# Kernel tuning notes

Hardware: AMD Instinct MI355X
Metric: run time of the kernel (lower is better)

Reference implementation:

```python
import jax, jax.numpy as jnp
import numpy as np

# Dimensions: D must equal C_CHUNK**2 (original code's view+transpose requires it)
D = 4096        # flattened input dim per sample
C_CHUNK = 64    # chunk_size (rows of G per chunk)
N_CHUNKS = D // C_CHUNK  # = 64
H = 512         # hidden dim of forward_func MLP
C_OUT = 8       # output classes of forward_func
B = 8           # batch size (state_batch has 2*B rows)
EPS_G = 1e-4    # metric regularizer (constant under grad)


def setup_inputs() -> dict:
    key = jax.random.key(0)
    ks = jax.random.split(key, 6)
    t = jax.random.uniform(ks[0], (1,), dtype=jnp.float32)
    state_batch = jax.random.normal(ks[1], (2 * B, D), dtype=jnp.float32)
    x0_batch = jax.random.normal(ks[2], (B, D), dtype=jnp.float32)
    x1_batch = jax.random.normal(ks[3], (B, D), dtype=jnp.float32)
    W1 = jax.random.normal(ks[4], (D, H), dtype=jnp.float32) / np.float32(np.sqrt(D))
    W2 = jax.random.normal(ks[5], (H, C_OUT), dtype=jnp.float32) / np.float32(np.sqrt(H))
    return {"t": t, "state_batch": state_batch, "x0_batch": x0_batch,
            "x1_batch": x1_batch, "W1": W1, "W2": W2}


def _accel_per_sample(x, v, W1, W2):
    """Chunked Christoffel-symbol contraction for one sample.
    x: [D] current point, v: [D] deviation velocity. Returns a: [D]."""
    def f(xi):  # forward_func: 2-layer tanh MLP, [D] -> [C_OUT]
        return jnp.tanh(xi @ W1) @ W2

    ones = jnp.ones((D,), x.dtype)

    def chunk_sums(xi):
        # G = J^T J + eps*I; row_sums[i] = sum_j G[i,j] computed without
        # materializing the D x D metric: J^T (J @ 1)  (+ const eps on diag).
        J = jax.jacrev(f)(xi)              # [C_OUT, D]
        row = J.T @ (J @ ones)             # [D]
        return row.reshape(N_CHUNKS, C_CHUNK).sum(axis=1)  # [N_CHUNKS]

    g = jax.jacrev(chunk_sums)(x)          # [N_CHUNKS, D] = dG_chunk_sum/dx
    g = g.reshape(N_CHUNKS, C_CHUNK, C_CHUNK)
    g = g / (jnp.linalg.norm(g, axis=2, keepdims=True) + 1e-6)
    Gamma = 0.5 * (g + jnp.swapaxes(g, 1, 2))   # symmetrized [nc, c, c]
    vc = v.reshape(N_CHUNKS, C_CHUNK)
    # a_chunk[i] = -sum_k Gamma[i,k] v_i v_k  (Christoffel quadratic in v)
    a = -jnp.einsum('nik,ni,nk->ni', Gamma, vc, vc)
    return a.reshape(D)


def reference(t, state_batch, x0_batch, x1_batch, W1, W2):
    ts = t[0]
    Bn = state_batch.shape[0] // 2
    deviation = state_batch[:Bn]
    dev_velocity = state_batch[Bn:]
    window = 4.0 * ts * (1.0 - ts)
    x = x0_batch + ts * (x1_batch - x0_batch) + window * deviation  # [B, D]
    a = jax.vmap(_accel_per_sample, in_axes=(0, 0, None, None))(x, dev_velocity, W1, W2)
    a = a / (jnp.linalg.norm(dev_velocity, axis=1, keepdims=True) + 1e-6)
    restoration = -0.1 * deviation
    return jnp.concatenate([dev_velocity, a + restoration], axis=0)  # [2B, D]
```

## Files before the change

kernel.cpp:

```cpp
#include <hip/hip_runtime.h>

#define D 4096
#define H 512
#define NCH 64
#define CCH 64
#define B 8

typedef __bf16 bf16x8 __attribute__((ext_vector_type(8)));
typedef float  f32x4  __attribute__((ext_vector_type(4)));

#define OFF_P    0
#define OFF_PHN  (OFF_P + NCH*H)
#define OFF_UPT  (OFF_PHN + H*NCH)
#define OFF_S    (OFF_UPT + B*H*NCH)
#define OFF_ST2  (OFF_S + B*H)
#define OFF_C    (OFF_ST2 + B*H)
#define OFF_MS   (OFF_C + H)
#define OFF_VN2  (OFF_MS + 64)
#define OFF_A1   (OFF_VN2 + 16)
#define OFF_ZB   (OFF_A1 + B*NCH*CCH)
#define OFF_W1H  (OFF_ZB + B*64*4096)
#define OFF_W1L  (OFF_W1H + (D*H)/2)
#define OFF_WH   (OFF_W1L + (D*H)/2)
#define OFF_WL   (OFF_WH + (B*NCH*H)/2)

__device__ __forceinline__ unsigned short f2bf(float x) {
    unsigned int u = __float_as_uint(x);
    unsigned int r = (u + 0x7FFFu + ((u >> 16) & 1u)) >> 16;
    return (unsigned short)r;
}
__device__ __forceinline__ float bf2f(unsigned short s) {
    return __uint_as_float(((unsigned int)s) << 16);
}

__global__ __launch_bounds__(256) void k1_reduce_w1(const float* __restrict__ W1,
                                                    const float* __restrict__ state,
                                                    const float* __restrict__ x0,
                                                    const float* __restrict__ x1,
                                                    const float* __restrict__ tptr,
                                                    float* __restrict__ ws) {
    int n   = blockIdx.x;
    int ht  = blockIdx.y;
    int tid = threadIdx.x;
    int hq  = ht * 32 + (tid & 31);
    int jh  = tid >> 5;

    __shared__ float xs[B][64];
    __shared__ f32x4 red[8][32][9];

    if (n == 0 && ht == 0 && tid < 80) ws[OFF_MS + tid] = 0.f;

    float ts = tptr[0];
    float window = 4.f * ts * (1.f - ts);
    if (tid < 64) {
        int d = n * 64 + tid;
        for (int b = 0; b < B; ++b) {
            float a0 = x0[b * D + d];
            float a1v = x1[b * D + d];
            float dev = state[b * D + d];
            xs[b][tid] = a0 + ts * (a1v - a0) + window * dev;
        }
    }
    __syncthreads();

    unsigned short* __restrict__ W1Hp = (unsigned short*)(ws + OFF_W1H);
    unsigned short* __restrict__ W1Lp = (unsigned short*)(ws + OFF_W1L);

    f32x4 p4 = {0.f, 0.f, 0.f, 0.f};
    f32x4 up[B];
#pragma unroll
    for (int b = 0; b < B; ++b) up[b] = p4;

#pragma unroll
    for (int jj = 0; jj < 8; ++jj) {
        int j = jh * 8 + jj;
        int d = n * 64 + j;
        f32x4 w = ((const f32x4*)W1)[d * (H / 4) + hq];
        p4 += w;
#pragma unroll
        for (int b = 0; b < B; ++b) up[b] += w * xs[b][j];
        unsigned short h0 = f2bf(w.x), h1 = f2bf(w.y), h2 = f2bf(w.z), h3 = f2bf(w.w);
        ushort4 hv = {h0, h1, h2, h3};
        ushort4 lv = {f2bf(w.x - bf2f(h0)), f2bf(w.y - bf2f(h1)),
                      f2bf(w.z - bf2f(h2)), f2bf(w.w - bf2f(h3))};
        *(ushort4*)(W1Hp + d * H + hq * 4) = hv;
        *(ushort4*)(W1Lp + d * H + hq * 4) = lv;
    }

    int l = tid & 31;
    red[jh][l][0] = p4;
#pragma unroll
    for (int b = 0; b < B; ++b) red[jh][l][1 + b] = up[b];
    __syncthreads();

    if (jh == 0) {
        f32x4 pt = red[0][l][0];
        f32x4 ut[B];
#pragma unroll
        for (int b = 0; b < B; ++b) ut[b] = red[0][l][1 + b];
        for (int g = 1; g < 8; ++g) {
            pt += red[g][l][0];
#pragma unroll
            for (int b = 0; b < B; ++b) ut[b] += red[g][l][1 + b];
        }
        *(f32x4*)(ws + OFF_P + n * H + hq * 4) = pt;
#pragma unroll
        for (int e = 0; e < 4; ++e) ws[OFF_PHN + (hq * 4 + e) * NCH + n] = pt[e];
#pragma unroll
        for (int b = 0; b < B; ++b)
#pragma unroll
            for (int e = 0; e < 4; ++e)
                ws[OFF_UPT + (b * H + hq * 4 + e) * NCH + n] = ut[b][e];
    }
}

__global__ __launch_bounds__(512) void k2_sample(const float* __restrict__ W2,
                                                 const float* __restrict__ state,
                                                 float* __restrict__ ws) {
    int hs = blockIdx.x;
    int b  = blockIdx.y;
    int tid = threadIdx.x;
    int hl  = tid >> 3;
    int jg  = tid & 7;
    int h   = hs * 64 + hl;
    int wv  = tid >> 6, ln = tid & 63;

    __shared__ float msp[8][8];
    __shared__ float lvp[8];

    const float* up = ws + OFF_UPT + (size_t)(b * H + h) * NCH + jg * 8;
    const float* pc = ws + OFF_PHN + (size_t)h * NCH + jg * 8;
    f32x4 ua = *(const f32x4*)up, ub = *(const f32x4*)(up + 4);
    f32x4 ca = *(const f32x4*)pc, cb = *(const f32x4*)(pc + 4);
    float u = ua.x+ua.y+ua.z+ua.w + ub.x+ub.y+ub.z+ub.w;
    float c = ca.x+ca.y+ca.z+ca.w + cb.x+cb.y+cb.z+cb.w;
    u += __shfl_xor(u, 1); u += __shfl_xor(u, 2); u += __shfl_xor(u, 4);
    c += __shfl_xor(c, 1); c += __shfl_xor(c, 2); c += __shfl_xor(c, 4);

    float tt  = tanhf(u);
    float s   = 1.f - tt * tt;
    float st2 = -2.f * tt * s;
    if (jg == 0) {
        ws[OFF_S   + b * H + h] = s;
        ws[OFF_ST2 + b * H + h] = st2;
        ws[OFF_C   + h] = c;
    }

    float mv = c * s * W2[hs * 512 + tid];
    mv += __shfl_xor(mv, 8); mv += __shfl_xor(mv, 16); mv += __shfl_xor(mv, 32);
    if (ln < 8) msp[wv][ln] = mv;

    float vv = state[(size_t)(B + b) * D + hs * 512 + tid];
    float v2 = vv * vv;
#pragma unroll
    for (int mk = 1; mk < 64; mk <<= 1) v2 += __shfl_xor(v2, mk);
    if (ln == 0) lvp[wv] = v2;
    __syncthreads();

    if (tid < 8) {
        float a = 0.f;
#pragma unroll
        for (int w = 0; w < 8; ++w) a += msp[w][tid];
        atomicAdd(&ws[OFF_MS + b * 8 + tid], a);
    }
    if (tid == 8) {
        float a = 0.f;
#pragma unroll
        for (int w = 0; w < 8; ++w) a += lvp[w];
        atomicAdd(&ws[OFF_VN2 + b], a);
    }
}

__global__ void k3_w(const float* __restrict__ W2,
                     float* __restrict__ ws) {
    int n = blockIdx.x, b = blockIdx.y, lane = threadIdx.x;
    float msv[8];
#pragma unroll
    for (int o = 0; o < 8; ++o) msv[o] = ws[OFF_MS + b * 8 + o];

    float M[8];
#pragma unroll
    for (int o = 0; o < 8; ++o) M[o] = 0.f;
#pragma unroll
    for (int j = 0; j < 8; ++j) {
        int h = j * 64 + lane;
        float ps = ws[OFF_P + n * H + h] * ws[OFF_S + b * H + h];
        const float4* wp = (const float4*)(W2 + h * 8);
        float4 wa = wp[0], wb = wp[1];
        M[0] += ps * wa.x; M[1] += ps * wa.y; M[2] += ps * wa.z; M[3] += ps * wa.w;
        M[4] += ps * wb.x; M[5] += ps * wb.y; M[6] += ps * wb.z; M[7] += ps * wb.w;
    }
#pragma unroll
    for (int mk = 1; mk < 64; mk <<= 1)
#pragma unroll
        for (int o = 0; o < 8; ++o) M[o] += __shfl_xor(M[o], mk);

    unsigned short* __restrict__ WHp = (unsigned short*)(ws + OFF_WH);
    unsigned short* __restrict__ WLp = (unsigned short*)(ws + OFF_WL);
#pragma unroll
    for (int j = 0; j < 8; ++j) {
        int h = j * 64 + lane;
        const float4* wp = (const float4*)(W2 + h * 8);
        float4 wa = wp[0], wb = wp[1];
        float r = wa.x*M[0] + wa.y*M[1] + wa.z*M[2] + wa.w*M[3]
                + wb.x*M[4] + wb.y*M[5] + wb.z*M[6] + wb.w*M[7];
        float q = wa.x*msv[0] + wa.y*msv[1] + wa.z*msv[2] + wa.w*msv[3]
                + wb.x*msv[4] + wb.y*msv[5] + wb.z*msv[6] + wb.w*msv[7];
        float P = ws[OFF_P + n * H + h];
        float wval = ws[OFF_ST2 + b * H + h] * (P * q + ws[OFF_C + h] * r);
        unsigned short hi = f2bf(wval);
        WHp[(b * NCH + n) * H + h] = hi;
        WLp[(b * NCH + n) * H + h] = f2bf(wval - bf2f(hi));
    }
}

__global__ __launch_bounds__(512, 2) void k4_mfma(const float* __restrict__ state,
                                                  float* __restrict__ ws) {
    int bid  = blockIdx.x;
    int tid  = threadIdx.x;
    int g    = tid >> 8;
    int gt   = tid & 255;
    int u    = bid * 2 + g;
    int i    = u >> 3, b = u & 7;
    int wvid = gt >> 6;
    int lane = tid & 63;
    int r16  = lane & 15;
    int kgrp = (lane >> 4) * 8;

    __shared__ float gp[2][2][64][67];
    __shared__ float coefs[2][64];

    const unsigned short* __restrict__ W1Hp = (const unsigned short*)(ws + OFF_W1H);
    const unsigned short* __restrict__ W1Lp = (const unsigned short*)(ws + OFF_W1L);
    const unsigned short* __restrict__ WHp  = (const unsigned short*)(ws + OFF_WH);
    const unsigned short* __restrict__ WLp  = (const unsigned short*)(ws + OFF_WL);

    f32x4 acc[4][4];
    f32x4 zz = {0.f, 0.f, 0.f, 0.f};
#pragma unroll
    for (int m = 0; m < 4; ++m)
#pragma unroll
        for (int c = 0; c < 4; ++c) acc[m][c] = zz;

    int kb    = wvid * 128 + kgrp;
    int baseA = (b * 64 + r16) * H;
    int baseB = (i * 64 + r16) * H;

    bf16x8 A0[8], B0[8], A1[8], B1[8];

#define LOADF(FA, FB, KOFS) do {                                           \
        int k_ = (KOFS);                                                   \
        _Pragma("unroll")                                                  \
        for (int m_ = 0; m_ < 4; ++m_) {                                   \
            int oA = baseA + m_ * 16 * H + k_;                             \
            FA[m_]     = *(const bf16x8*)(WHp + oA);                       \
            FA[4 + m_] = *(const bf16x8*)(WLp + oA);                       \
            int oB = baseB + m_ * 16 * H + k_;                             \
            FB[m_]     = *(const bf16x8*)(W1Hp + oB);                      \
            FB[4 + m_] = *(const bf16x8*)(W1Lp + oB);                      \
        } } while (0)

#define MFMA12(FA, FB) do {                                                \
        _Pragma("unroll")                                                  \
        for (int m = 0; m < 4; ++m)                                        \
        _Pragma("unroll")                                                  \
        for (int c = 0; c < 4; ++c) {                                      \
            acc[m][c] = __builtin_amdgcn_mfma_f32_16x16x32_bf16(FA[m], FB[c], acc[m][c], 0, 0, 0);       \
            acc[m][c] = __builtin_amdgcn_mfma_f32_16x16x32_bf16(FA[m], FB[4 + c], acc[m][c], 0, 0, 0);   \
            acc[m][c] = __builtin_amdgcn_mfma_f32_16x16x32_bf16(FA[4 + m], FB[c], acc[m][c], 0, 0, 0);   \
        } } while (0)

    LOADF(A0, B0, kb);
    LOADF(A1, B1, kb + 32);
    MFMA12(A0, B0);
    LOADF(A0, B0, kb + 64);
    MFMA12(A1, B1);
    LOADF(A1, B1, kb + 96);
    MFMA12(A0, B0);
    MFMA12(A1, B1);

#undef LOADF
#undef MFMA12

    int rowb = (lane >> 4) * 4;
    if (wvid < 2) {
        float (*gpp)[67] = gp[g][wvid];
#pragma unroll
        for (int m = 0; m < 4; ++m)
#pragma unroll
            for (int c = 0; c < 4; ++c)
#pragma unroll
                for (int e = 0; e < 4; ++e)
                    gpp[m * 16 + rowb + e][c * 16 + r16] = acc[m][c][e];
    }
    __syncthreads();
    if (wvid >= 2) {
        float (*gpp)[67] = gp[g][wvid - 2];
#pragma unroll
        for (int m = 0; m < 4; ++m)
#pragma unroll
            for (int c = 0; c < 4; ++c)
#pragma unroll
                for (int e = 0; e < 4; ++e)
                    gpp[m * 16 + rowb + e][c * 16 + r16] += acc[m][c][e];
    }
    __syncthreads();

    const float* v = state + (size_t)(B + b) * D;
    if (gt < 64) {
        int n = gt;
        float ss = 0.f, y = 0.f;
#pragma unroll 8
        for (int k = 0; k < 64; ++k) {
            float gv = gp[g][0][n][k] + gp[g][1][n][k];
            ss += gv * gv;
            y  += gv * v[n * 64 + k];
        }
        float nrm = sqrtf(ss) + 1e-6f;
        ws[OFF_A1 + (size_t)(b * NCH + n) * CCH + i] = y / nrm;
        coefs[g][n] = v[n * 64 + i] / nrm;
    }
    __syncthreads();

    float* zb = ws + OFF_ZB + ((size_t)b * 64 + i) * 4096;
#pragma unroll
    for (int r = 0; r < 16; ++r) {
        int idx = gt + r * 256;
        int n = idx >> 6, k = idx & 63;
        zb[idx] = (gp[g][0][n][k] + gp[g][1][n][k]) * coefs[g][n];
    }
}

__global__ void k5_final(const float* __restrict__ state,
                         const float* __restrict__ ws,
                         float* __restrict__ out) {
    int idx = blockIdx.x * 512 + threadIdx.x;
    float vel = state[32768 + idx];
    out[idx] = vel;
    int b = idx >> 12, e = idx & 4095;
    const float* zb = ws + OFF_ZB + (size_t)b * 64 * 4096 + e;
    float z = 0.f;
#pragma unroll 8
    for (int i = 0; i < 64; ++i) z += zb[(size_t)i * 4096];
    float a1 = ws[OFF_A1 + (size_t)b * 4096 + e];
    float vn = sqrtf(ws[OFF_VN2 + b]) + 1e-6f;
    float av = -0.5f * vel * (a1 + z) / vn;
    out[32768 + idx] = av - 0.1f * state[idx];
}

extern "C" void kernel_launch(void* const* d_in, const int* in_sizes, int n_in,
                              void* d_out, int out_size, void* d_ws, size_t ws_size,
                              hipStream_t stream) {
    const float* t   = (const float*)d_in[0];
    const float* st  = (const float*)d_in[1];
    const float* x0  = (const float*)d_in[2];
    const float* x1  = (const float*)d_in[3];
    const float* W1  = (const float*)d_in[4];
    const float* W2  = (const float*)d_in[5];
    float* out = (float*)d_out;
    float* ws  = (float*)d_ws;

    hipLaunchKernelGGL(k1_reduce_w1, dim3(64, 4), dim3(256), 0, stream, W1, st, x0, x1, t, ws);
    hipLaunchKernelGGL(k2_sample,    dim3(8, 8),  dim3(512), 0, stream, W2, st, ws);
    hipLaunchKernelGGL(k3_w,         dim3(64, 8), dim3(64),  0, stream, W2, ws);
    hipLaunchKernelGGL(k4_mfma,      dim3(256),   dim3(512), 0, stream, st, ws);
    hipLaunchKernelGGL(k5_final,     dim3(64),    dim3(512), 0, stream, st, ws, out);
}
```

Baseline: 117.8 us.

## Fold k2 into k1 via atomic reductions and recompute tanh terms in k3

Removes the k2_sample kernel. k1 now accumulates the per-hidden sums c and u with atomicAdd and also computes the velocity norm, and k3 recomputes tanh, s and the M/Q projections itself instead of reading precomputed values. k1 runs twice as many blocks at half the width, and a memset replaces the in-kernel zeroing. This also switches the bf16 split to compiler conversions. It saves one launch and the transposed partial-sum writes, at the cost of many atomics and redundant tanh work repeated across the 64 chunk blocks in k3.

New measurement: 122.0 us. +3.5%, slower.

```diff
diff --git a/kernel.cpp b/kernel.cpp
--- a/kernel.cpp
+++ b/kernel.cpp
@@ -10,13 +10,9 @@
 typedef float  f32x4  __attribute__((ext_vector_type(4)));
 
 #define OFF_P    0
-#define OFF_PHN  (OFF_P + NCH*H)
-#define OFF_UPT  (OFF_PHN + H*NCH)
-#define OFF_S    (OFF_UPT + B*H*NCH)
-#define OFF_ST2  (OFF_S + B*H)
-#define OFF_C    (OFF_ST2 + B*H)
-#define OFF_MS   (OFF_C + H)
-#define OFF_VN2  (OFF_MS + 64)
+#define OFF_C    (OFF_P + NCH*H)
+#define OFF_U    (OFF_C + H)
+#define OFF_VN2  (OFF_U + B*H)
 #define OFF_A1   (OFF_VN2 + 16)
 #define OFF_ZB   (OFF_A1 + B*NCH*CCH)
 #define OFF_W1H  (OFF_ZB + B*64*4096)
@@ -24,16 +20,16 @@
 #define OFF_WH   (OFF_W1L + (D*H)/2)
 #define OFF_WL   (OFF_WH + (B*NCH*H)/2)
 
-__device__ __forceinline__ unsigned short f2bf(float x) {
-    unsigned int u = __float_as_uint(x);
-    unsigned int r = (u + 0x7FFFu + ((u >> 16) & 1u)) >> 16;
-    return (unsigned short)r;
-}
-__device__ __forceinline__ float bf2f(unsigned short s) {
-    return __uint_as_float(((unsigned int)s) << 16);
-}
-
-__global__ __launch_bounds__(256) void k1_reduce_w1(const float* __restrict__ W1,
+__device__ __forceinline__ unsigned short bfbits(float x) {
+    union { __bf16 b; unsigned short u; } cv;
+    cv.b = (__bf16)x;
+    return cv.u;
+}
+__device__ __forceinline__ float bfval(float x) {
+    return (float)(__bf16)x;
+}
+
+__global__ __launch_bounds__(128) void k1_reduce_w1(const float* __restrict__ W1,
                                                     const float* __restrict__ state,
                                                     const float* __restrict__ x0,
                                                     const float* __restrict__ x1,
@@ -42,13 +38,11 @@
     int n   = blockIdx.x;
     int ht  = blockIdx.y;
     int tid = threadIdx.x;
-    int hq  = ht * 32 + (tid & 31);
-    int jh  = tid >> 5;
+    int hq  = ht * 16 + (tid & 15);
+    int jh  = tid >> 4;
 
     __shared__ float xs[B][64];
-    __shared__ f32x4 red[8][32][9];
-
-    if (n == 0 && ht == 0 && tid < 80) ws[OFF_MS + tid] = 0.f;
+    __shared__ f32x4 red[8][16][9];
 
     float ts = tptr[0];
     float window = 4.f * ts * (1.f - ts);
@@ -79,21 +73,28 @@
         p4 += w;
 #pragma unroll
         for (int b = 0; b < B; ++b) up[b] += w * xs[b][j];
-        unsigned short h0 = f2bf(w.x), h1 = f2bf(w.y), h2 = f2bf(w.z), h3 = f2bf(w.w);
-        ushort4 hv = {h0, h1, h2, h3};
-        ushort4 lv = {f2bf(w.x - bf2f(h0)), f2bf(w.y - bf2f(h1)),
-                      f2bf(w.z - bf2f(h2)), f2bf(w.w - bf2f(h3))};
+        ushort4 hv = {bfbits(w.x), bfbits(w.y), bfbits(w.z), bfbits(w.w)};
+        ushort4 lv = {bfbits(w.x - bfval(w.x)), bfbits(w.y - bfval(w.y)),
+                      bfbits(w.z - bfval(w.z)), bfbits(w.w - bfval(w.w))};
         *(ushort4*)(W1Hp + d * H + hq * 4) = hv;
         *(ushort4*)(W1Lp + d * H + hq * 4) = lv;
     }
 
-    int l = tid & 31;
+    if (tid < 64) {
+        float vv = state[(size_t)(B + ht) * D + n * 64 + tid];
+        float v2 = vv * vv;
+#pragma unroll
+        for (int mk = 1; mk < 64; mk <<= 1) v2 += __shfl_xor(v2, mk);
+        if (tid == 0) atomicAdd(&ws[OFF_VN2 + ht], v2);
+    }
+
+    int l = tid & 15;
     red[jh][l][0] = p4;
 #pragma unroll
     for (int b = 0; b < B; ++b) red[jh][l][1 + b] = up[b];
     __syncthreads();
 
-    if (jh == 0) {
+    if (tid < 16) {
         f32x4 pt = red[0][l][0];
         f32x4 ut[B];
 #pragma unroll
@@ -105,95 +106,46 @@
         }
         *(f32x4*)(ws + OFF_P + n * H + hq * 4) = pt;
 #pragma unroll
-        for (int e = 0; e < 4; ++e) ws[OFF_PHN + (hq * 4 + e) * NCH + n] = pt[e];
+        for (int e = 0; e < 4; ++e) atomicAdd(&ws[OFF_C + hq * 4 + e], pt[e]);
 #pragma unroll
         for (int b = 0; b < B; ++b)
 #pragma unroll
             for (int e = 0; e < 4; ++e)
-                ws[OFF_UPT + (b * H + hq * 4 + e) * NCH + n] = ut[b][e];
-    }
-}
-
-__global__ __launch_bounds__(512) void k2_sample(const float* __restrict__ W2,
-                                                 const float* __restrict__ state,
-                                                 float* __restrict__ ws) {
-    int hs = blockIdx.x;
-    int b  = blockIdx.y;
-    int tid = threadIdx.x;
-    int hl  = tid >> 3;
-    int jg  = tid & 7;
-    int h   = hs * 64 + hl;
-    int wv  = tid >> 6, ln = tid & 63;
-
-    __shared__ float msp[8][8];
-    __shared__ float lvp[8];
-
-    const float* up = ws + OFF_UPT + (size_t)(b * H + h) * NCH + jg * 8;
-    const float* pc = ws + OFF_PHN + (size_t)h * NCH + jg * 8;
-    f32x4 ua = *(const f32x4*)up, ub = *(const f32x4*)(up + 4);
-    f32x4 ca = *(const f32x4*)pc, cb = *(const f32x4*)(pc + 4);
-    float u = ua.x+ua.y+ua.z+ua.w + ub.x+ub.y+ub.z+ub.w;
-    float c = ca.x+ca.y+ca.z+ca.w + cb.x+cb.y+cb.z+cb.w;
-    u += __shfl_xor(u, 1); u += __shfl_xor(u, 2); u += __shfl_xor(u, 4);
-    c += __shfl_xor(c, 1); c += __shfl_xor(c, 2); c += __shfl_xor(c, 4);
-
-    float tt  = tanhf(u);
-    float s   = 1.f - tt * tt;
-    float st2 = -2.f * tt * s;
-    if (jg == 0) {
-        ws[OFF_S   + b * H + h] = s;
-        ws[OFF_ST2 + b * H + h] = st2;
-        ws[OFF_C   + h] = c;
-    }
-
-    float mv = c * s * W2[hs * 512 + tid];
-    mv += __shfl_xor(mv, 8); mv += __shfl_xor(mv, 16); mv += __shfl_xor(mv, 32);
-    if (ln < 8) msp[wv][ln] = mv;
-
-    float vv = state[(size_t)(B + b) * D + hs * 512 + tid];
-    float v2 = vv * vv;
-#pragma unroll
-    for (int mk = 1; mk < 64; mk <<= 1) v2 += __shfl_xor(v2, mk);
-    if (ln == 0) lvp[wv] = v2;
-    __syncthreads();
-
-    if (tid < 8) {
-        float a = 0.f;
-#pragma unroll
-        for (int w = 0; w < 8; ++w) a += msp[w][tid];
-        atomicAdd(&ws[OFF_MS + b * 8 + tid], a);
-    }
-    if (tid == 8) {
-        float a = 0.f;
-#pragma unroll
-        for (int w = 0; w < 8; ++w) a += lvp[w];
-        atomicAdd(&ws[OFF_VN2 + b], a);
+                atomicAdd(&ws[OFF_U + b * H + hq * 4 + e], ut[b][e]);
     }
 }
 
 __global__ void k3_w(const float* __restrict__ W2,
                      float* __restrict__ ws) {
     int n = blockIdx.x, b = blockIdx.y, lane = threadIdx.x;
-    float msv[8];
-#pragma unroll
-    for (int o = 0; o < 8; ++o) msv[o] = ws[OFF_MS + b * 8 + o];
-
-    float M[8];
-#pragma unroll
-    for (int o = 0; o < 8; ++o) M[o] = 0.f;
+    float M[8], Q[8], s2j[8];
+#pragma unroll
+    for (int o = 0; o < 8; ++o) { M[o] = 0.f; Q[o] = 0.f; }
+
 #pragma unroll
     for (int j = 0; j < 8; ++j) {
         int h = j * 64 + lane;
-        float ps = ws[OFF_P + n * H + h] * ws[OFF_S + b * H + h];
+        float u  = ws[OFF_U + b * H + h];
+        float tt = tanhf(u);
+        float s  = 1.f - tt * tt;
+        s2j[j]   = -2.f * tt * s;
+        float c  = ws[OFF_C + h];
+        float P  = ws[OFF_P + n * H + h];
+        float ps = P * s, cs = c * s;
         const float4* wp = (const float4*)(W2 + h * 8);
         float4 wa = wp[0], wb = wp[1];
         M[0] += ps * wa.x; M[1] += ps * wa.y; M[2] += ps * wa.z; M[3] += ps * wa.w;
         M[4] += ps * wb.x; M[5] += ps * wb.y; M[6] += ps * wb.z; M[7] += ps * wb.w;
+        Q[0] += cs * wa.x; Q[1] += cs * wa.y; Q[2] += cs * wa.z; Q[3] += cs * wa.w;
+        Q[4] += cs * wb.x; Q[5] += cs * wb.y; Q[6] += cs * wb.z; Q[7] += cs * wb.w;
     }
 #pragma unroll
     for (int mk = 1; mk < 64; mk <<= 1)
 #pragma unroll
-        for (int o = 0; o < 8; ++o) M[o] += __shfl_xor(M[o], mk);
+        for (int o = 0; o < 8; ++o) {
+            M[o] += __shfl_xor(M[o], mk);
+            Q[o] += __shfl_xor(Q[o], mk);
+        }
 
     unsigned short* __restrict__ WHp = (unsigned short*)(ws + OFF_WH);
     unsigned short* __restrict__ WLp = (unsigned short*)(ws + OFF_WL);
@@ -204,13 +156,13 @@
         float4 wa = wp[0], wb = wp[1];
         float r = wa.x*M[0] + wa.y*M[1] + wa.z*M[2] + wa.w*M[3]
                 + wb.x*M[4] + wb.y*M[5] + wb.z*M[6] + wb.w*M[7];
-        float q = wa.x*msv[0] + wa.y*msv[1] + wa.z*msv[2] + wa.w*msv[3]
-                + wb.x*msv[4] + wb.y*msv[5] + wb.z*msv[6] + wb.w*msv[7];
+        float q = wa.x*Q[0] + wa.y*Q[1] + wa.z*Q[2] + wa.w*Q[3]
+                + wb.x*Q[4] + wb.y*Q[5] + wb.z*Q[6] + wb.w*Q[7];
         float P = ws[OFF_P + n * H + h];
-        float wval = ws[OFF_ST2 + b * H + h] * (P * q + ws[OFF_C + h] * r);
-        unsigned short hi = f2bf(wval);
-        WHp[(b * NCH + n) * H + h] = hi;
-        WLp[(b * NCH + n) * H + h] = f2bf(wval - bf2f(hi));
+        float c = ws[OFF_C + h];
+        float wval = s2j[j] * (P * q + c * r);
+        WHp[(b * NCH + n) * H + h] = bfbits(wval);
+        WLp[(b * NCH + n) * H + h] = bfbits(wval - bfval(wval));
     }
 }
 
@@ -360,8 +312,8 @@
     float* out = (float*)d_out;
     float* ws  = (float*)d_ws;
 
-    hipLaunchKernelGGL(k1_reduce_w1, dim3(64, 4), dim3(256), 0, stream, W1, st, x0, x1, t, ws);
-    hipLaunchKernelGGL(k2_sample,    dim3(8, 8),  dim3(512), 0, stream, W2, st, ws);
+    hipMemsetAsync(ws + OFF_C, 0, (H + B * H + 16) * sizeof(float), stream);
+    hipLaunchKernelGGL(k1_reduce_w1, dim3(64, 8), dim3(128), 0, stream, W1, st, x0, x1, t, ws);
     hipLaunchKernelGGL(k3_w,         dim3(64, 8), dim3(64),  0, stream, W2, ws);
     hipLaunchKernelGGL(k4_mfma,      dim3(256),   dim3(512), 0, stream, st, ws);
     hipLaunchKernelGGL(k5_final,     dim3(64),    dim3(512), 0, stream, st, ws, out);
```
